# Kernel tuning notes

Hardware: AMD Instinct MI355X
Metric: run time of the kernel (lower is better)

## Reference

```python
import jax, jax.numpy as jnp
import numpy as np

K = 16
EPS = 1e-5

def _conv1x1(w, b, x):
    # w: [O, I], x: [B, I, N] -> [B, O, N]
    return jnp.einsum('oi,bin->bon', w, x) + b[None, :, None]

def _bn(g, be, m, v, x):
    # inference-mode batchnorm over channel dim of [B, C, N]
    inv = g / jnp.sqrt(v + EPS)
    return x * inv[None, :, None] + (be - m * inv)[None, :, None]

def setup_inputs() -> dict:
    key = jax.random.key(0)
    ks = jax.random.split(key, 16)
    B, C, N = 2, 128, 8192
    d = {}
    d['x'] = jax.random.normal(ks[0], (B, C, N), jnp.float32)
    d['xyz'] = jax.random.normal(ks[1], (B, N, 3), jnp.float32)
    def conv(k, o, i):
        k1, k2 = jax.random.split(k)
        s = 1.0 / np.sqrt(i)
        return (jax.random.uniform(k1, (o, i), jnp.float32, -s, s),
                jax.random.uniform(k2, (o,), jnp.float32, -s, s))
    def bn(k, c):
        return (jax.random.uniform(k, (c,), jnp.float32, 0.5, 1.5),
                jnp.zeros((c,), jnp.float32), jnp.zeros((c,), jnp.float32), jnp.ones((c,), jnp.float32))
    # boundary_net: 2C->C (bn,relu), C->C (bn,relu)
    d['bw1'], d['bb1'] = conv(ks[2], C, 2 * C)
    d['bn1g'], d['bn1b'], d['bn1m'], d['bn1v'] = bn(ks[3], C)
    d['bw2'], d['bb2'] = conv(ks[4], C, C)
    d['bn2g'], d['bn2b'], d['bn2m'], d['bn2v'] = bn(ks[5], C)
    # spatial_relation: 4->32 (bn,relu), 32->64
    d['sw1'], d['sb1'] = conv(ks[6], 32, 4)
    d['sbng'], d['sbnb'], d['sbnm'], d['sbnv'] = bn(ks[7], 32)
    d['sw2'], d['sb2'] = conv(ks[8], 64, 32)
    # attention: C+64 -> C//2 (bn,relu), C//2 -> C, sigmoid
    d['aw1'], d['ab1'] = conv(ks[9], C // 2, C + 64)
    d['abng'], d['abnb'], d['abnm'], d['abnv'] = bn(ks[10], C // 2)
    d['aw2'], d['ab2'] = conv(ks[11], C, C // 2)
    return d

def reference(x, xyz, bw1, bb1, bn1g, bn1b, bn1m, bn1v, bw2, bb2, bn2g, bn2b, bn2m, bn2v,
              sw1, sb1, sbng, sbnb, sbnm, sbnv, sw2, sb2,
              aw1, ab1, abng, abnb, abnm, abnv, aw2, ab2):
    B, C, N = x.shape
    # pairwise squared distances [B, N, N]
    xx = jnp.sum(xyz * xyz, axis=2)  # [B, N]
    dist = xx[:, :, None] + xx[:, None, :] - 2.0 * jnp.einsum('bnd,bmd->bnm', xyz, xyz)
    _, knn_idx = jax.lax.top_k(-dist, K)  # [B, N, K], K smallest distances
    # gather neighbor coords [B, N, K, 3]
    knn_xyz = jax.vmap(lambda p, i: p[i])(xyz, knn_idx)
    rel = knn_xyz - xyz[:, :, None, :]                  # [B, N, K, 3]
    rel_d = jnp.sqrt(jnp.sum(rel * rel, axis=-1))       # [B, N, K]
    mean_rel = jnp.mean(rel, axis=2).transpose(0, 2, 1)   # [B, 3, N]
    mean_d = jnp.mean(rel_d, axis=2)[:, None, :]           # [B, 1, N]
    spatial = jnp.concatenate([mean_rel, mean_d], axis=1)  # [B, 4, N]
    s = jax.nn.relu(_bn(sbng, sbnb, sbnm, sbnv, _conv1x1(sw1, sb1, spatial)))
    spatial_feat = _conv1x1(sw2, sb2, s)  # [B, 64, N]
    # gather neighbor features [B, C, N, K]
    knn_feat = jax.vmap(lambda xb, ib: xb[:, ib])(x, knn_idx)
    max_diff = jnp.max(knn_feat - x[:, :, :, None], axis=3)  # [B, C, N]
    bf = jnp.concatenate([x, max_diff], axis=1)  # [B, 2C, N]
    bf = jax.nn.relu(_bn(bn1g, bn1b, bn1m, bn1v, _conv1x1(bw1, bb1, bf)))
    boundary_feat = jax.nn.relu(_bn(bn2g, bn2b, bn2m, bn2v, _conv1x1(bw2, bb2, bf)))
    ai = jnp.concatenate([x, spatial_feat], axis=1)  # [B, C+64, N]
    a = jax.nn.relu(_bn(abng, abnb, abnm, abnv, _conv1x1(aw1, ab1, ai)))
    attn = jax.nn.sigmoid(_conv1x1(aw2, ab2, a))  # [B, C, N]
    return x + boundary_feat * attn
```

## Files before the change

kernel.cpp:

```cpp
#include <hip/hip_runtime.h>
#include <math.h>

#define NPTS  8192
#define NB    2
#define NTOT  (NPTS*NB)
#define GD    60
#define NCELL (GD*GD*GD)
#define TOTC  (NB*NCELL)
#define HCELL 0.2f
#define INVH  5.0f
#define ORGN  (-6.0f)
#define NN    8192
#define SCAN_CHUNK 1024
#define NBLK_SCAN  ((TOTC + SCAN_CHUNK - 1) / SCAN_CHUNK)
#define RSTART    2
#define RESC      4
#define SEL_CAP  1024

#define OFF_CNT     ((size_t)0)
#define OFF_OFFS    (OFF_CNT    + (size_t)TOTC*4)
#define OFF_CELLID  (OFF_OFFS   + (size_t)TOTC*4)
#define OFF_RANK    (OFF_CELLID + (size_t)NTOT*4)
#define OFF_SPOS    (OFF_RANK   + (size_t)NTOT*4)
#define OFF_KNN     (OFF_SPOS   + (size_t)NTOT*16)
#define OFF_SPATIAL (OFF_KNN    + (size_t)NTOT*16*4)
#define OFF_XT      (OFF_SPATIAL+ (size_t)NB*4*NPTS*4)
#define OFF_MD      (OFF_XT     + (size_t)NB*128*NPTS*4)
#define OFF_S1      (OFF_MD     + (size_t)NB*128*NPTS*4)
#define OFF_SF      (OFF_S1     + (size_t)NB*32*NPTS*4)
#define OFF_Y1      (OFF_SF     + (size_t)NB*64*NPTS*4)
#define OFF_Y2      (OFF_Y1     + (size_t)NB*128*NPTS*4)
#define OFF_A1      (OFF_Y2     + (size_t)NB*128*NPTS*4)
#define OFF_SC      (OFF_A1     + (size_t)NB*64*NPTS*4)
#define OFF_BSUM    (OFF_SC     + (size_t)1088*4)
#define OFF_BPRE    (OFF_BSUM   + (size_t)NBLK_SCAN*4)
#define OFF_RNG     (((OFF_BPRE + (size_t)NBLK_SCAN*4) + 15) & ~(size_t)15)

static __device__ __forceinline__ float sumsq3(float x, float y, float z) {
    return __fadd_rn(__fadd_rn(__fmul_rn(x, x), __fmul_rn(y, y)), __fmul_rn(z, z));
}
static __device__ __forceinline__ float pdist4(float qx, float qy, float qz, float qxx,
                                               float px, float py, float pz) {
    float pxx = sumsq3(px, py, pz);
    float dot = __fadd_rn(__fadd_rn(__fmul_rn(qx, px), __fmul_rn(qy, py)), __fmul_rn(qz, pz));
    return __fsub_rn(__fadd_rn(qxx, pxx), __fadd_rn(dot, dot));
}
static __device__ __forceinline__ unsigned fkey(float f) {
    unsigned b = __float_as_uint(f);
    return b ^ ((unsigned)(((int)b) >> 31) | 0x80000000u);
}
static __device__ __forceinline__ unsigned long long shflx64(unsigned long long v, int m) {
    unsigned lo = __shfl_xor((unsigned)v, m, 64);
    unsigned hi = __shfl_xor((unsigned)(v >> 32), m, 64);
    return ((unsigned long long)hi << 32) | lo;
}
static __device__ __forceinline__ int wave_scan_incl(int v, int lane) {
    #pragma unroll
    for (int d = 1; d < 64; d <<= 1) {
        int u = __shfl_up(v, d, 64);
        v += (lane >= d) ? u : 0;
    }
    return v;
}
static __device__ __forceinline__ unsigned long long tkmake(float m) {
    return ((unsigned long long)(fkey(__fsub_rn(__fmul_rn(m, m), 1e-4f)) + 1u)) << 27;
}

__global__ void cell_build(const float* __restrict__ xyz, int* __restrict__ cnt,
                           int* __restrict__ cellid, int* __restrict__ rank) {
    int t = blockIdx.x * 256 + threadIdx.x;
    if (t >= NTOT) return;
    const float* p = xyz + (size_t)t * 3;
    float x = p[0], y = p[1], z = p[2];
    int cx = min(GD - 1, max(0, (int)floorf((x - ORGN) * INVH)));
    int cy = min(GD - 1, max(0, (int)floorf((y - ORGN) * INVH)));
    int cz = min(GD - 1, max(0, (int)floorf((z - ORGN) * INVH)));
    int gcell = (t >> 13) * NCELL + (cz * GD + cy) * GD + cx;
    rank[t] = atomicAdd(&cnt[gcell], 1);
    cellid[t] = gcell;
}

__global__ __launch_bounds__(256) void scan_sums(const int* __restrict__ cnt, int* __restrict__ bsum) {
    __shared__ int red[256];
    int blk = blockIdx.x, t = threadIdx.x;
    int i0 = blk * SCAN_CHUNK + t * 4;
    int s = 0;
    if (i0 + 3 < TOTC) {
        int4 v = *(const int4*)(cnt + i0);
        s = v.x + v.y + v.z + v.w;
    } else {
        for (int j = 0; j < 4; ++j) if (i0 + j < TOTC) s += cnt[i0 + j];
    }
    red[t] = s;
    __syncthreads();
    for (int d = 128; d > 0; d >>= 1) {
        if (t < d) red[t] += red[t + d];
        __syncthreads();
    }
    if (t == 0) bsum[blk] = red[0];
}

__global__ __launch_bounds__(512) void scan_top(const int* __restrict__ bsum, int* __restrict__ bpre) {
    __shared__ int ps[512];
    int t = threadIdx.x;
    int v = (t < NBLK_SCAN) ? bsum[t] : 0;
    ps[t] = v;
    __syncthreads();
    for (int d = 1; d < 512; d <<= 1) {
        int u = 0;
        if (t >= d) u = ps[t - d];
        __syncthreads();
        ps[t] += u;
        __syncthreads();
    }
    if (t < NBLK_SCAN) bpre[t] = ps[t] - v;
}

__global__ __launch_bounds__(256) void scan_write(const int* __restrict__ cnt, const int* __restrict__ bpre,
                                                  int* __restrict__ offs, int2* __restrict__ rng) {
    __shared__ int ps[256];
    int blk = blockIdx.x, t = threadIdx.x;
    int i0 = blk * SCAN_CHUNK + t * 4;
    int a = 0, b = 0, c = 0, d = 0;
    if (i0 + 3 < TOTC) {
        int4 v = *(const int4*)(cnt + i0);
        a = v.x; b = v.y; c = v.z; d = v.w;
    } else {
        if (i0 + 0 < TOTC) a = cnt[i0 + 0];
        if (i0 + 1 < TOTC) b = cnt[i0 + 1];
        if (i0 + 2 < TOTC) c = cnt[i0 + 2];
        if (i0 + 3 < TOTC) d = cnt[i0 + 3];
    }
    int s = a + b + c + d;
    ps[t] = s;
    __syncthreads();
    for (int dd = 1; dd < 256; dd <<= 1) {
        int u = 0;
        if (t >= dd) u = ps[t - dd];
        __syncthreads();
        ps[t] += u;
        __syncthreads();
    }
    int base = bpre[blk] + ps[t] - s;
    if (i0 + 3 < TOTC) {
        offs[i0 + 0] = base;
        offs[i0 + 1] = base + a;
        offs[i0 + 2] = base + a + b;
        offs[i0 + 3] = base + a + b + c;
        *(int4*)(rng + i0)     = make_int4(base, base + a, base + a, base + a + b);
        *(int4*)(rng + i0 + 2) = make_int4(base + a + b, base + a + b + c,
                                           base + a + b + c, base + s);
    } else {
        if (i0 + 0 < TOTC) { offs[i0 + 0] = base;             rng[i0 + 0] = make_int2(base, base + a); }
        if (i0 + 1 < TOTC) { offs[i0 + 1] = base + a;         rng[i0 + 1] = make_int2(base + a, base + a + b); }
        if (i0 + 2 < TOTC) { offs[i0 + 2] = base + a + b;     rng[i0 + 2] = make_int2(base + a + b, base + a + b + c); }
        if (i0 + 3 < TOTC) { offs[i0 + 3] = base + a + b + c; rng[i0 + 3] = make_int2(base + a + b + c, base + s); }
    }
}

__global__ void scatter_k(const float* __restrict__ xyz, const int* __restrict__ cellid,
                          const int* __restrict__ rank, const int* __restrict__ offs,
                          float4* __restrict__ spos) {
    int t = blockIdx.x * 256 + threadIdx.x;
    if (t >= NTOT) return;
    const float* p = xyz + (size_t)t * 3;
    float x = p[0], y = p[1], z = p[2];
    int pos = offs[cellid[t]] + rank[t];
    spos[pos] = make_float4(x, y, z, __int_as_float(t & (NPTS - 1)));
}

__global__ __launch_bounds__(64) void knn_kernel(const float4* __restrict__ spos,
                                                 const int2* __restrict__ rng,
                                                 int* __restrict__ knn,
                                                 float* __restrict__ spatial) {
    __shared__ __align__(16) unsigned long long sel[SEL_CAP];
    __shared__ __align__(16) unsigned long long sel2[512];
    int lane = threadIdx.x;
    int bid  = blockIdx.x;
    int s = (bid & 7) * (NTOT / 8) + (bid >> 3);
    float4 q = spos[s];
    float qx = q.x, qy = q.y, qz = q.z;
    float qxx = sumsq3(qx, qy, qz);
    int b  = s >> 13;
    int nq = __float_as_int(q.w);
    int cx = min(GD - 1, max(0, (int)floorf((qx - ORGN) * INVH)));
    int cy = min(GD - 1, max(0, (int)floorf((qy - ORGN) * INVH)));
    int cz = min(GD - 1, max(0, (int)floorf((qz - ORGN) * INVH)));
    const int2* rg = rng + b * NCELL;

    float mlx = qx - (ORGN + (float)cx * HCELL);
    float mhx = (ORGN + (float)(cx + 1) * HCELL) - qx;
    float mly = qy - (ORGN + (float)cy * HCELL);
    float mhy = (ORGN + (float)(cy + 1) * HCELL) - qy;
    float mlz = qz - (ORGN + (float)cz * HCELL);
    float mhz = (ORGN + (float)(cz + 1) * HCELL) - qz;
    float margin0 = fminf(fminf(fminf(mlx, mhx), fminf(mly, mhy)), fminf(mlz, mhz));

    int tot = 0, ovf = 0;

    auto scan_ball = [&](int RB, float mfin, unsigned long long tkfin) {
        if (mfin <= 0.f) return;
        float mfin2 = mfin * mfin;
        int L = 2 * RB + 1, nrows = L * L;
        for (int r0 = 0; r0 < nrows; r0 += 64) {
            int nr = min(64, nrows - r0);
            int rr = r0 + lane;
            int num = 0, start = 0;
            if (rr < nrows) {
                int dzr = rr / L - RB, dyr = rr % L - RB;
                int zc = cz + dzr, yc = cy + dyr;
                if ((unsigned)zc < GD && (unsigned)yc < GD) {
                    float ylo = ORGN + (float)yc * HCELL;
                    float zlo = ORGN + (float)zc * HCELL;
                    float dyl = fmaxf(fmaxf(ylo - qy, qy - (ylo + HCELL)), 0.f);
                    float dzl = fmaxf(fmaxf(zlo - qz, qz - (zlo + HCELL)), 0.f);
                    float rem = mfin2 - dyl * dyl - dzl * dzl;
                    if (rem > -1e-4f) {
                        float xh = sqrtf(fmaxf(rem, 0.f)) + 1e-3f;
                        int xlo = max(0, (int)floorf((qx - xh - ORGN) * INVH));
                        int xhi = min(GD - 1, (int)floorf((qx + xh - ORGN) * INVH));
                        if (xlo <= xhi) {
                            int rowb = (zc * GD + yc) * GD;
                            start = rg[rowb + xlo].x;
                            num   = rg[rowb + xhi].y - start;
                        }
                    }
                }
            }
            int inc = wave_scan_incl(num, lane);
            int ctot = __shfl(inc, 63, 64);
            if (ctot == 0) continue;
            int excl = inc - num;
            auto eg = [&](int base, int& sv, float4& pv, bool& vld) {
                int t = base + lane;
                vld = t < ctot;
                int tc = vld ? t : (ctot - 1);
                int lo = 0, hi = nr - 1;
                #pragma unroll
                for (int st = 0; st < 6; ++st) {
                    int mid = (lo + hi + 1) >> 1;
                    int e = __shfl(excl, mid, 64);
                    bool g = (e <= tc);
                    lo = g ? mid : lo;
                    hi = g ? hi : (mid - 1);
                }
                sv = __shfl(start, lo, 64) + (tc - __shfl(excl, lo, 64));
                pv = spos[sv];
            };
            int s0; float4 p0; bool v0;
            eg(0, s0, p0, v0);
            for (int base = 0; base < ctot; base += 64) {
                int s1 = 0; float4 p1 = p0; bool v1 = false;
                if (base + 64 < ctot) eg(base + 64, s1, p1, v1);
                float d = pdist4(qx, qy, qz, qxx, p0.x, p0.y, p0.z);
                unsigned long long key = ((unsigned long long)fkey(d) << 27)
                                       | ((unsigned long long)(unsigned)__float_as_int(p0.w) << 14)
                                       | (unsigned)s0;
                bool pass = v0 && (key < tkfin);
                unsigned long long mk = __ballot(pass);
                int cnum = (int)__popcll(mk);
                if (tot + cnum > SEL_CAP) { ovf = 1; return; }
                if (pass) sel[tot + (int)__popcll(mk & ((1ULL << lane) - 1ULL))] = key;
                tot += cnum;
                s0 = s1; p0 = p1; v0 = v1;
            }
        }
    };

    auto count_below = [&](unsigned long long tk) {
        int c = 0;
        for (int t0 = 0; t0 < tot; t0 += 64) {
            int tt = t0 + lane;
            if (tt < tot) c += (sel[tt] < tk) ? 1 : 0;
        }
        for (int o = 32; o > 0; o >>= 1) c += __shfl_xor(c, o, 64);
        return c;
    };

    float mfin1 = margin0 + (float)RSTART * HCELL;
    unsigned long long tkf1 = (mfin1 > 0.f) ? tkmake(mfin1) : 0ULL;
    if (tkf1) scan_ball(RSTART, mfin1, tkf1);

    unsigned long long tkey_sel = ~0ULL;
    int csel = 0;
    bool have = false;
    if (!ovf && tot >= 16) {
        float mA = margin0 + 1.0f * HCELL;
        if (mA > 0.f) {
            unsigned long long tkA = tkmake(mA);
            int cA = count_below(tkA);
            if (cA >= 16) { tkey_sel = tkA; csel = cA; have = true; }
        }
        if (!have) { tkey_sel = ~0ULL; csel = tot; have = true; }
    }
    if (!have && !ovf) {
        tot = 0;
        float mfin4 = margin0 + (float)RESC * HCELL;
        unsigned long long tkf4 = (mfin4 > 0.f) ? tkmake(mfin4) : 0ULL;
        if (tkf4) scan_ball(RESC, mfin4, tkf4);
        if (!ovf && tot >= 16) {
            float mB = margin0 + (float)(RESC - 1) * HCELL;
            if (mB > 0.f) {
                unsigned long long tkB = tkmake(mB);
                int cB = count_below(tkB);
                if (cB >= 16) { tkey_sel = tkB; csel = cB; have = true; }
            }
            if (!have) { tkey_sel = ~0ULL; csel = tot; have = true; }
        }
    }

    if (!have) {
        const float LADR[16] = {0.35f, 0.4725f, 0.637875f, 0.86113125f,
                                1.1625272f, 1.5694117f, 2.1187058f, 2.8602529f,
                                3.8613414f, 5.2128109f, 7.0372947f, 9.5003478f,
                                12.825470f, 17.314384f, 23.374418f, 31.555464f};
        int sbase = b << 13;
        int cc[16];
        #pragma unroll
        for (int k = 0; k < 16; ++k) cc[k] = 0;
        for (int i0 = 0; i0 < NPTS; i0 += 64) {
            float4 p = spos[sbase + i0 + lane];
            float d = pdist4(qx, qy, qz, qxx, p.x, p.y, p.z);
            #pragma unroll
            for (int k = 0; k < 16; ++k) cc[k] += (d < LADR[k] * LADR[k]) ? 1 : 0;
        }
        #pragma unroll
        for (int k = 0; k < 16; ++k)
            for (int o = 32; o > 0; o >>= 1) cc[k] += __shfl_xor(cc[k], o, 64);
        float Tq = LADR[15] * LADR[15]; int cL = cc[15];
        #pragma unroll
        for (int k = 14; k >= 0; --k) if (cc[k] >= 16) { Tq = LADR[k] * LADR[k]; cL = cc[k]; }
        if (cL <= SEL_CAP) {
            tot = 0;
            for (int i0 = 0; i0 < NPTS; i0 += 64) {
                int idx = sbase + i0 + lane;
                float4 p = spos[idx];
                float d = pdist4(qx, qy, qz, qxx, p.x, p.y, p.z);
                bool pass = (d < Tq);
                unsigned long long key = ((unsigned long long)fkey(d) << 27)
                                       | ((unsigned long long)(unsigned)__float_as_int(p.w) << 14)
                                       | (unsigned)idx;
                unsigned long long mk = __ballot(pass);
                if (pass) sel[tot + (int)__popcll(mk & ((1ULL << lane) - 1ULL))] = key;
                tot += (int)__popcll(mk);
            }
            tkey_sel = ~0ULL;
            csel = tot;
        } else {
            unsigned long long* mybuf = sel + lane;
            unsigned long long minkey = ~0ULL, maxkey = 0;
            int nbuf = 0;
            for (int i = lane; i < NPTS; i += 64) {
                float4 p = spos[sbase + i];
                float d = pdist4(qx, qy, qz, qxx, p.x, p.y, p.z);
                unsigned long long key = ((unsigned long long)fkey(d) << 27)
                                       | ((unsigned long long)(unsigned)__float_as_int(p.w) << 14)
                                       | (unsigned)(sbase + i);
                if (nbuf < 16) {
                    mybuf[(size_t)nbuf * 64] = key;
                    ++nbuf;
                    minkey = (key < minkey) ? key : minkey;
                    maxkey = (key > maxkey) ? key : maxkey;
                } else if (key < maxkey) {
                    unsigned long long vmax = 0, v2 = 0;
                    int pmax = 0;
                    #pragma unroll
                    for (int j = 0; j < 16; ++j) {
                        unsigned long long v = mybuf[(size_t)j * 64];
                        if (v > vmax) { v2 = vmax; vmax = v; pmax = j; }
                        else if (v > v2) { v2 = v; }
                    }
                    mybuf[(size_t)pmax * 64] = key;
                    maxkey = (key > v2) ? key : v2;
                    minkey = (key < minkey) ? key : minkey;
                }
            }
            unsigned long long keep = ~0ULL;
            for (int k = 0; k < 16; ++k) {
                unsigned long long m = minkey;
                for (int o = 32; o > 0; o >>= 1) {
                    unsigned long long pv = shflx64(m, o);
                    m = (pv < m) ? pv : m;
                }
                unsigned long long bal = __ballot(minkey == m);
                int wl = __ffsll((long long)bal) - 1;
                if (lane == wl) {
                    int pos = 0;
                    for (int j = 0; j < nbuf; ++j) if (mybuf[(size_t)j * 64] == m) pos = j;
                    --nbuf;
                    mybuf[(size_t)pos * 64] = mybuf[(size_t)nbuf * 64];
                    unsigned long long nm = ~0ULL;
                    for (int j = 0; j < nbuf; ++j) {
                        unsigned long long v = mybuf[(size_t)j * 64];
                        nm = (v < nm) ? v : nm;
                    }
                    minkey = nm;
                }
                if (lane == k) keep = m;
            }
            float rx = 0.f, ry = 0.f, rz = 0.f, rd = 0.f;
            if (lane < 16) {
                int sp = (int)(keep & 0x3FFFu);
                int oi = (int)((keep >> 14) & 0x1FFFu);
                float4 p = spos[sp];
                rx = p.x - qx; ry = p.y - qy; rz = p.z - qz;
                rd = sqrtf(__fadd_rn(__fadd_rn(__fmul_rn(rx, rx), __fmul_rn(ry, ry)), __fmul_rn(rz, rz)));
                knn[(((size_t)b << 13) + nq) * 16 + lane] = oi;
            }
            for (int o = 8; o > 0; o >>= 1) {
                rx += __shfl_xor(rx, o, 64);
                ry += __shfl_xor(ry, o, 64);
                rz += __shfl_xor(rz, o, 64);
                rd += __shfl_xor(rd, o, 64);
            }
            if (lane == 0) {
                const float inv16 = 0.0625f;
                spatial[((size_t)b * 4 + 0) * NPTS + nq] = rx * inv16;
                spatial[((size_t)b * 4 + 1) * NPTS + nq] = ry * inv16;
                spatial[((size_t)b * 4 + 2) * NPTS + nq] = rz * inv16;
                spatial[((size_t)b * 4 + 3) * NPTS + nq] = rd * inv16;
            }
            return;
        }
    }

    const unsigned long long* src = sel;
    int m = tot;
    if (tkey_sel != ~0ULL && csel <= 512) {
        int w = 0;
        for (int t0 = 0; t0 < tot; t0 += 64) {
            int tt = t0 + lane;
            unsigned long long v = (tt < tot) ? sel[tt] : ~0ULL;
            bool pass = (tt < tot) && (v < tkey_sel);
            unsigned long long mk = __ballot(pass);
            if (pass) sel2[w + (int)__popcll(mk & ((1ULL << lane) - 1ULL))] = v;
            w += (int)__popcll(mk);
        }
        asm volatile("s_waitcnt lgkmcnt(0)" ::: "memory");
        __builtin_amdgcn_sched_barrier(0);
        src = sel2; m = w;
        tkey_sel = ~0ULL;
    }
    float rxs = 0.f, rys = 0.f, rzs = 0.f, rds = 0.f;
    for (int t0 = 0; t0 < m; t0 += 64) {
        int tt = t0 + lane;
        if (tt < m) {
            unsigned long long kt = src[tt];
            if (kt < tkey_sel) {
                int rr = 0;
                for (int j = 0; j < m; ++j) rr += (src[j] < kt) ? 1 : 0;
                if (rr < 16) {
                    int sp = (int)(kt & 0x3FFFu);
                    int oi = (int)((kt >> 14) & 0x1FFFu);
                    float4 p = spos[sp];
                    float dx = p.x - qx, dy = p.y - qy, dz = p.z - qz;
                    float dl = sqrtf(__fadd_rn(__fadd_rn(__fmul_rn(dx, dx), __fmul_rn(dy, dy)), __fmul_rn(dz, dz)));
                    knn[(((size_t)b << 13) + nq) * 16 + rr] = oi;
                    rxs += dx; rys += dy; rzs += dz; rds += dl;
                }
            }
        }
    }
    for (int o = 32; o > 0; o >>= 1) {
        rxs += __shfl_xor(rxs, o, 64);
        rys += __shfl_xor(rys, o, 64);
        rzs += __shfl_xor(rzs, o, 64);
        rds += __shfl_xor(rds, o, 64);
    }
    if (lane == 0) {
        const float inv16 = 0.0625f;
        spatial[((size_t)b * 4 + 0) * NPTS + nq] = rxs * inv16;
        spatial[((size_t)b * 4 + 1) * NPTS + nq] = rys * inv16;
        spatial[((size_t)b * 4 + 2) * NPTS + nq] = rzs * inv16;
        spatial[((size_t)b * 4 + 3) * NPTS + nq] = rds * inv16;
    }
}

__global__ void transpose_k(const float* __restrict__ x, float* __restrict__ xT) {
    __shared__ float tl[32][33];
    int b = blockIdx.z;
    int n0 = blockIdx.x * 32, c0 = blockIdx.y * 32;
    int tx = threadIdx.x, ty = threadIdx.y;
    const float* xb = x + (size_t)b * 128 * NN;
    float* xtb = xT + (size_t)b * NN * 128;
    for (int i = 0; i < 32; i += 8) tl[ty + i][tx] = xb[(size_t)(c0 + ty + i) * NN + n0 + tx];
    __syncthreads();
    for (int i = 0; i < 32; i += 8) xtb[(size_t)(n0 + ty + i) * 128 + c0 + tx] = tl[tx][ty + i];
}

__global__ __launch_bounds__(256) void md_k(const float* __restrict__ xT,
                                            const int* __restrict__ knn,
                                            float* __restrict__ md) {
    __shared__ int ki[8][16];
    __shared__ float smd[8][132];
    int b = blockIdx.y;
    int n0 = blockIdx.x * 8;
    int tid = threadIdx.x;
    if (tid < 128) ki[tid >> 4][tid & 15] = knn[(((size_t)b << 13) + n0 + (tid >> 4)) * 16 + (tid & 15)];
    __syncthreads();
    int nl = tid >> 5;
    int c4 = (tid & 31) * 4;
    const float* xb = xT + (size_t)b * NPTS * 128;
    float4 m = make_float4(-3.0e38f, -3.0e38f, -3.0e38f, -3.0e38f);
    #pragma unroll
    for (int k = 0; k < 16; ++k) {
        const float4 g = *(const float4*)(xb + (size_t)ki[nl][k] * 128 + c4);
        m.x = fmaxf(m.x, g.x); m.y = fmaxf(m.y, g.y); m.z = fmaxf(m.z, g.z); m.w = fmaxf(m.w, g.w);
    }
    const float4 own = *(const float4*)(xb + (size_t)(n0 + nl) * 128 + c4);
    m.x -= own.x; m.y -= own.y; m.z -= own.z; m.w -= own.w;
    *(float4*)(&smd[nl][c4]) = m;
    __syncthreads();
    for (int r = 0; r < 4; ++r) {
        int c = (tid >> 3) + 32 * r;
        int n2 = tid & 7;
        md[((size_t)b * 128 + c) * NN + n0 + n2] = smd[n2][c];
    }
}

__global__ void prep_k(const float* bb1, const float* g1, const float* be1, const float* m1, const float* v1,
                       const float* bb2, const float* g2, const float* be2, const float* m2, const float* v2,
                       const float* sb1, const float* gs,  const float* bes, const float* ms, const float* vs,
                       const float* sb2,
                       const float* ab1, const float* ga,  const float* bea, const float* ma, const float* va,
                       const float* ab2, float* sc) {
    int t = threadIdx.x;
    if (t < 128) {
        float i1 = g1[t] / sqrtf(v1[t] + 1e-5f);
        sc[t] = i1;        sc[128 + t] = bb1[t] * i1 + be1[t] - m1[t] * i1;
        float i2 = g2[t] / sqrtf(v2[t] + 1e-5f);
        sc[256 + t] = i2;  sc[384 + t] = bb2[t] * i2 + be2[t] - m2[t] * i2;
        sc[832 + t] = 1.0f; sc[960 + t] = ab2[t];
    }
    if (t < 32) {
        float is = gs[t] / sqrtf(vs[t] + 1e-5f);
        sc[512 + t] = is;  sc[544 + t] = sb1[t] * is + bes[t] - ms[t] * is;
    }
    if (t < 64) {
        sc[576 + t] = 1.0f; sc[640 + t] = sb2[t];
        float ia = ga[t] / sqrtf(va[t] + 1e-5f);
        sc[704 + t] = ia;  sc[768 + t] = ab1[t] * ia + bea[t] - ma[t] * ia;
    }
}

template <int O, int K, int TILE_N, int SPLIT, int ACT>
__global__ __launch_bounds__(256) void conv_bn(const float* __restrict__ srcA,
                                               const float* __restrict__ srcB,
                                               const float* __restrict__ W,
                                               const float* __restrict__ scale,
                                               const float* __restrict__ shift,
                                               float* __restrict__ out,
                                               const float* __restrict__ resx,
                                               const float* __restrict__ y2,
                                               float* __restrict__ dout) {
    constexpr int KC  = (K < 64) ? K : 64;
    constexpr int NT4 = TILE_N / 4;
    constexpr int O4  = O / 4;
    static_assert(NT4 * O4 == 256, "thread mapping");
    __shared__ float wT[KC][O + 4];
    __shared__ float inT[KC][TILE_N];
    int tid = threadIdx.x;
    int b = blockIdx.z;
    int n0 = blockIdx.x * TILE_N;
    int n_thr = tid % NT4;
    int o_thr = tid / NT4;
    float acc[4][4] = {{0.f, 0.f, 0.f, 0.f}, {0.f, 0.f, 0.f, 0.f}, {0.f, 0.f, 0.f, 0.f}, {0.f, 0.f, 0.f, 0.f}};

    for (int k0 = 0; k0 < K; k0 += KC) {
        for (int idx = tid; idx < KC * O; idx += 256) {
            int cc = idx % KC;
            int o  = idx / KC;
            wT[cc][o] = W[(size_t)o * K + k0 + cc];
        }
        for (int idx = tid; idx < KC * NT4; idx += 256) {
            int cc = idx / NT4;
            int nf = idx % NT4;
            int cg = k0 + cc;
            const float* src = (cg < SPLIT)
                ? (srcA + ((size_t)b * SPLIT + cg) * NN)
                : (srcB + ((size_t)b * (K - SPLIT) + (cg - SPLIT)) * NN);
            *(float4*)(&inT[cc][nf * 4]) = *(const float4*)(src + n0 + nf * 4);
        }
        __syncthreads();
        #pragma unroll 8
        for (int c = 0; c < KC; ++c) {
            float4 wv = *(const float4*)(&wT[c][o_thr * 4]);
            float4 iv = *(const float4*)(&inT[c][n_thr * 4]);
            acc[0][0] = fmaf(wv.x, iv.x, acc[0][0]); acc[0][1] = fmaf(wv.x, iv.y, acc[0][1]);
            acc[0][2] = fmaf(wv.x, iv.z, acc[0][2]); acc[0][3] = fmaf(wv.x, iv.w, acc[0][3]);
            acc[1][0] = fmaf(wv.y, iv.x, acc[1][0]); acc[1][1] = fmaf(wv.y, iv.y, acc[1][1]);
            acc[1][2] = fmaf(wv.y, iv.z, acc[1][2]); acc[1][3] = fmaf(wv.y, iv.w, acc[1][3]);
            acc[2][0] = fmaf(wv.z, iv.x, acc[2][0]); acc[2][1] = fmaf(wv.z, iv.y, acc[2][1]);
            acc[2][2] = fmaf(wv.z, iv.z, acc[2][2]); acc[2][3] = fmaf(wv.z, iv.w, acc[2][3]);
            acc[3][0] = fmaf(wv.w, iv.x, acc[3][0]); acc[3][1] = fmaf(wv.w, iv.y, acc[3][1]);
            acc[3][2] = fmaf(wv.w, iv.z, acc[3][2]); acc[3][3] = fmaf(wv.w, iv.w, acc[3][3]);
        }
        __syncthreads();
    }
    #pragma unroll
    for (int j = 0; j < 4; ++j) {
        int o = o_thr * 4 + j;
        float scv = scale[o], shv = shift[o];
        float4 v;
        v.x = fmaf(acc[j][0], scv, shv);
        v.y = fmaf(acc[j][1], scv, shv);
        v.z = fmaf(acc[j][2], scv, shv);
        v.w = fmaf(acc[j][3], scv, shv);
        size_t obase = ((size_t)b * O + o) * NN + n0 + n_thr * 4;
        if (ACT == 1) {
            v.x = fmaxf(v.x, 0.f); v.y = fmaxf(v.y, 0.f); v.z = fmaxf(v.z, 0.f); v.w = fmaxf(v.w, 0.f);
            *(float4*)(out + obase) = v;
        } else if (ACT == 2) {
            float4 xr = *(const float4*)(resx + obase);
            float4 yr = *(const float4*)(y2 + obase);
            v.x = xr.x + yr.x / (1.f + __expf(-v.x));
            v.y = xr.y + yr.y / (1.f + __expf(-v.y));
            v.z = xr.z + yr.z / (1.f + __expf(-v.z));
            v.w = xr.w + yr.w / (1.f + __expf(-v.w));
            *(float4*)(dout + obase) = v;
        } else {
            *(float4*)(out + obase) = v;
        }
    }
}

extern "C" void kernel_launch(void* const* d_in, const int* in_sizes, int n_in,
                              void* d_out, int out_size, void* d_ws, size_t ws_size,
                              hipStream_t stream) {
    (void)in_sizes; (void)n_in; (void)out_size; (void)ws_size;
    const float* x    = (const float*)d_in[0];
    const float* xyz  = (const float*)d_in[1];
    const float* bw1  = (const float*)d_in[2];
    const float* bb1  = (const float*)d_in[3];
    const float* bn1g = (const float*)d_in[4];
    const float* bn1b = (const float*)d_in[5];
    const float* bn1m = (const float*)d_in[6];
    const float* bn1v = (const float*)d_in[7];
    const float* bw2  = (const float*)d_in[8];
    const float* bb2  = (const float*)d_in[9];
    const float* bn2g = (const float*)d_in[10];
    const float* bn2b = (const float*)d_in[11];
    const float* bn2m = (const float*)d_in[12];
    const float* bn2v = (const float*)d_in[13];
    const float* sw1  = (const float*)d_in[14];
    const float* sb1  = (const float*)d_in[15];
    const float* sbng = (const float*)d_in[16];
    const float* sbnb = (const float*)d_in[17];
    const float* sbnm = (const float*)d_in[18];
    const float* sbnv = (const float*)d_in[19];
    const float* sw2  = (const float*)d_in[20];
    const float* sb2  = (const float*)d_in[21];
    const float* aw1  = (const float*)d_in[22];
    const float* ab1  = (const float*)d_in[23];
    const float* abng = (const float*)d_in[24];
    const float* abnb = (const float*)d_in[25];
    const float* abnm = (const float*)d_in[26];
    const float* abnv = (const float*)d_in[27];
    const float* aw2  = (const float*)d_in[28];
    const float* ab2  = (const float*)d_in[29];

    char* ws = (char*)d_ws;
    int*    cnt    = (int*)(ws + OFF_CNT);
    int*    offs   = (int*)(ws + OFF_OFFS);
    int*    cellid = (int*)(ws + OFF_CELLID);
    int*    rank   = (int*)(ws + OFF_RANK);
    float4* spos   = (float4*)(ws + OFF_SPOS);
    int*    knn    = (int*)(ws + OFF_KNN);
    float*  spat   = (float*)(ws + OFF_SPATIAL);
    float*  xT     = (float*)(ws + OFF_XT);
    float*  md     = (float*)(ws + OFF_MD);
    float*  s1b    = (float*)(ws + OFF_S1);
    float*  sfb    = (float*)(ws + OFF_SF);
    float*  y1b    = (float*)(ws + OFF_Y1);
    float*  y2b    = (float*)(ws + OFF_Y2);
    float*  a1b    = (float*)(ws + OFF_A1);
    float*  sc     = (float*)(ws + OFF_SC);
    int*    bsum   = (int*)(ws + OFF_BSUM);
    int*    bpre   = (int*)(ws + OFF_BPRE);
    int2*   rng    = (int2*)(ws + OFF_RNG);
    float*  dout   = (float*)d_out;

    hipMemsetAsync(cnt, 0, (size_t)TOTC * 4, stream);
    cell_build<<<dim3((NTOT + 255) / 256), 256, 0, stream>>>(xyz, cnt, cellid, rank);
    scan_sums<<<dim3(NBLK_SCAN), 256, 0, stream>>>(cnt, bsum);
    scan_top<<<dim3(1), 512, 0, stream>>>(bsum, bpre);
    scan_write<<<dim3(NBLK_SCAN), 256, 0, stream>>>(cnt, bpre, offs, rng);
    scatter_k<<<dim3((NTOT + 255) / 256), 256, 0, stream>>>(xyz, cellid, rank, offs, spos);
    knn_kernel<<<dim3(NTOT), 64, 0, stream>>>(spos, rng, knn, spat);
    transpose_k<<<dim3(NPTS / 32, 128 / 32, NB), dim3(32, 8), 0, stream>>>(x, xT);
    md_k<<<dim3(NPTS / 8, NB), 256, 0, stream>>>(xT, knn, md);
    prep_k<<<1, 128, 0, stream>>>(bb1, bn1g, bn1b, bn1m, bn1v,
                                  bb2, bn2g, bn2b, bn2m, bn2v,
                                  sb1, sbng, sbnb, sbnm, sbnv,
                                  sb2,
                                  ab1, abng, abnb, abnm, abnv,
                                  ab2, sc);
    conv_bn<32, 4, 128, 4, 1><<<dim3(NPTS / 128, 1, NB), 256, 0, stream>>>(
        spat, spat, sw1, sc + 512, sc + 544, s1b, nullptr, nullptr, nullptr);
    conv_bn<64, 32, 64, 32, 0><<<dim3(NPTS / 64, 1, NB), 256, 0, stream>>>(
        s1b, s1b, sw2, sc + 576, sc + 640, sfb, nullptr, nullptr, nullptr);
    conv_bn<128, 256, 32, 128, 1><<<dim3(NPTS / 32, 1, NB), 256, 0, stream>>>(
        x, md, bw1, sc + 0, sc + 128, y1b, nullptr, nullptr, nullptr);
    conv_bn<128, 128, 32, 128, 1><<<dim3(NPTS / 32, 1, NB), 256, 0, stream>>>(
        y1b, y1b, bw2, sc + 256, sc + 384, y2b, nullptr, nullptr, nullptr);
    conv_bn<64, 192, 64, 128, 1><<<dim3(NPTS / 64, 1, NB), 256, 0, stream>>>(
        x, sfb, aw1, sc + 704, sc + 768, a1b, nullptr, nullptr, nullptr);
    conv_bn<128, 64, 32, 64, 2><<<dim3(NPTS / 32, 1, NB), 256, 0, stream>>>(
        a1b, a1b, aw2, sc + 832, sc + 960, dout, x, y2b, dout);
}
```

Before: 326.0 us.

## Make knn kernel persistent and batch neighbor-cell loads four chunks at a time

The knn kernel becomes a grid-stride persistent loop over queries with a fixed 4096-block grid, replacing one block per query. Candidate loads are batched four 64-wide chunks at once to raise memory-level parallelism. The count of keys below the tighter threshold is now accumulated during the scan, removing a separate count_below pass over shared memory. The sel2 buffer is halved to 256 to cut shared memory and allow more resident waves, at the cost of a lower cutoff for the compaction step.

```diff
diff --git a/kernel.cpp b/kernel.cpp
--- a/kernel.cpp
+++ b/kernel.cpp
@@ -16,6 +16,7 @@
 #define RSTART    2
 #define RESC      4
 #define SEL_CAP  1024
+#define GRID_KNN 4096
 
 #define OFF_CNT     ((size_t)0)
 #define OFF_OFFS    (OFF_CNT    + (size_t)TOTC*4)
@@ -174,305 +175,312 @@
                                                  int* __restrict__ knn,
                                                  float* __restrict__ spatial) {
     __shared__ __align__(16) unsigned long long sel[SEL_CAP];
-    __shared__ __align__(16) unsigned long long sel2[512];
+    __shared__ __align__(16) unsigned long long sel2[256];
     int lane = threadIdx.x;
-    int bid  = blockIdx.x;
-    int s = (bid & 7) * (NTOT / 8) + (bid >> 3);
-    float4 q = spos[s];
-    float qx = q.x, qy = q.y, qz = q.z;
-    float qxx = sumsq3(qx, qy, qz);
-    int b  = s >> 13;
-    int nq = __float_as_int(q.w);
-    int cx = min(GD - 1, max(0, (int)floorf((qx - ORGN) * INVH)));
-    int cy = min(GD - 1, max(0, (int)floorf((qy - ORGN) * INVH)));
-    int cz = min(GD - 1, max(0, (int)floorf((qz - ORGN) * INVH)));
-    const int2* rg = rng + b * NCELL;
-
-    float mlx = qx - (ORGN + (float)cx * HCELL);
-    float mhx = (ORGN + (float)(cx + 1) * HCELL) - qx;
-    float mly = qy - (ORGN + (float)cy * HCELL);
-    float mhy = (ORGN + (float)(cy + 1) * HCELL) - qy;
-    float mlz = qz - (ORGN + (float)cz * HCELL);
-    float mhz = (ORGN + (float)(cz + 1) * HCELL) - qz;
-    float margin0 = fminf(fminf(fminf(mlx, mhx), fminf(mly, mhy)), fminf(mlz, mhz));
-
-    int tot = 0, ovf = 0;
-
-    auto scan_ball = [&](int RB, float mfin, unsigned long long tkfin) {
-        if (mfin <= 0.f) return;
-        float mfin2 = mfin * mfin;
-        int L = 2 * RB + 1, nrows = L * L;
-        for (int r0 = 0; r0 < nrows; r0 += 64) {
-            int nr = min(64, nrows - r0);
-            int rr = r0 + lane;
-            int num = 0, start = 0;
-            if (rr < nrows) {
-                int dzr = rr / L - RB, dyr = rr % L - RB;
-                int zc = cz + dzr, yc = cy + dyr;
-                if ((unsigned)zc < GD && (unsigned)yc < GD) {
-                    float ylo = ORGN + (float)yc * HCELL;
-                    float zlo = ORGN + (float)zc * HCELL;
-                    float dyl = fmaxf(fmaxf(ylo - qy, qy - (ylo + HCELL)), 0.f);
-                    float dzl = fmaxf(fmaxf(zlo - qz, qz - (zlo + HCELL)), 0.f);
-                    float rem = mfin2 - dyl * dyl - dzl * dzl;
-                    if (rem > -1e-4f) {
-                        float xh = sqrtf(fmaxf(rem, 0.f)) + 1e-3f;
-                        int xlo = max(0, (int)floorf((qx - xh - ORGN) * INVH));
-                        int xhi = min(GD - 1, (int)floorf((qx + xh - ORGN) * INVH));
-                        if (xlo <= xhi) {
-                            int rowb = (zc * GD + yc) * GD;
-                            start = rg[rowb + xlo].x;
-                            num   = rg[rowb + xhi].y - start;
+    for (int qi = blockIdx.x; qi < NTOT; qi += gridDim.x) {
+        int s = (qi & 7) * (NTOT / 8) + (qi >> 3);
+        float4 q = spos[s];
+        float qx = q.x, qy = q.y, qz = q.z;
+        float qxx = sumsq3(qx, qy, qz);
+        int b  = s >> 13;
+        int nq = __float_as_int(q.w);
+        int cx = min(GD - 1, max(0, (int)floorf((qx - ORGN) * INVH)));
+        int cy = min(GD - 1, max(0, (int)floorf((qy - ORGN) * INVH)));
+        int cz = min(GD - 1, max(0, (int)floorf((qz - ORGN) * INVH)));
+        const int2* rg = rng + b * NCELL;
+
+        float mlx = qx - (ORGN + (float)cx * HCELL);
+        float mhx = (ORGN + (float)(cx + 1) * HCELL) - qx;
+        float mly = qy - (ORGN + (float)cy * HCELL);
+        float mhy = (ORGN + (float)(cy + 1) * HCELL) - qy;
+        float mlz = qz - (ORGN + (float)cz * HCELL);
+        float mhz = (ORGN + (float)(cz + 1) * HCELL) - qz;
+        float margin0 = fminf(fminf(fminf(mlx, mhx), fminf(mly, mhy)), fminf(mlz, mhz));
+
+        int tot = 0, ovf = 0, cA = 0;
+        unsigned long long g_tkfin = 0, g_tkA = 0;
+
+        auto scan_ball = [&](int RB, float mfin) {
+            float mfin2 = mfin * mfin;
+            int L = 2 * RB + 1, nrows = L * L;
+            for (int r0 = 0; r0 < nrows && !ovf; r0 += 64) {
+                int nr = min(64, nrows - r0);
+                int rr = r0 + lane;
+                int num = 0, start = 0;
+                if (rr < nrows) {
+                    int dzr = rr / L - RB, dyr = rr % L - RB;
+                    int zc = cz + dzr, yc = cy + dyr;
+                    if ((unsigned)zc < GD && (unsigned)yc < GD) {
+                        float ylo = ORGN + (float)yc * HCELL;
+                        float zlo = ORGN + (float)zc * HCELL;
+                        float dyl = fmaxf(fmaxf(ylo - qy, qy - (ylo + HCELL)), 0.f);
+                        float dzl = fmaxf(fmaxf(zlo - qz, qz - (zlo + HCELL)), 0.f);
+                        float rem = mfin2 - dyl * dyl - dzl * dzl;
+                        if (rem > -1e-4f) {
+                            float xh = sqrtf(fmaxf(rem, 0.f)) + 1e-3f;
+                            int xlo = max(0, (int)floorf((qx - xh - ORGN) * INVH));
+                            int xhi = min(GD - 1, (int)floorf((qx + xh - ORGN) * INVH));
+                            if (xlo <= xhi) {
+                                int rowb = (zc * GD + yc) * GD;
+                                start = rg[rowb + xlo].x;
+                                num   = rg[rowb + xhi].y - start;
+                            }
                         }
                     }
                 }
+                int inc = wave_scan_incl(num, lane);
+                int ctot = __shfl(inc, 63, 64);
+                if (ctot == 0) continue;
+                int excl = inc - num;
+                int nch = (ctot + 63) >> 6;
+                auto srch = [&](int ck, int& sv, bool& vld) {
+                    int t = ck * 64 + lane;
+                    vld = t < ctot;
+                    int tc = vld ? t : (ctot - 1);
+                    int lo = 0, hi = nr - 1;
+                    #pragma unroll
+                    for (int st = 0; st < 6; ++st) {
+                        int mid = (lo + hi + 1) >> 1;
+                        int e = __shfl(excl, mid, 64);
+                        bool g = (e <= tc);
+                        lo = g ? mid : lo;
+                        hi = g ? hi : mid - 1;
+                    }
+                    sv = __shfl(start, lo, 64) + (tc - __shfl(excl, lo, 64));
+                };
+                auto proc = [&](int sv, float4 pv, bool vld) {
+                    if (ovf) return;
+                    float d = pdist4(qx, qy, qz, qxx, pv.x, pv.y, pv.z);
+                    unsigned long long key = ((unsigned long long)fkey(d) << 27)
+                                           | ((unsigned long long)(unsigned)__float_as_int(pv.w) << 14)
+                                           | (unsigned)sv;
+                    bool pass = vld && (key < g_tkfin);
+                    unsigned long long mk = __ballot(pass);
+                    int cnum = (int)__popcll(mk);
+                    if (tot + cnum > SEL_CAP) { ovf = 1; return; }
+                    if (pass) sel[tot + (int)__popcll(mk & ((1ULL << lane) - 1ULL))] = key;
+                    cA += (pass && key < g_tkA) ? 1 : 0;
+                    tot += cnum;
+                };
+                for (int cb = 0; cb < nch; cb += 4) {
+                    int s0 = 0, s1 = 0, s2 = 0, s3 = 0;
+                    bool v0 = false, v1 = false, v2 = false, v3 = false;
+                    float4 p0 = make_float4(0.f, 0.f, 0.f, 0.f);
+                    float4 p1 = p0, p2 = p0, p3 = p0;
+                    srch(cb, s0, v0); p0 = spos[s0];
+                    if (cb + 1 < nch) { srch(cb + 1, s1, v1); p1 = spos[s1]; }
+                    if (cb + 2 < nch) { srch(cb + 2, s2, v2); p2 = spos[s2]; }
+                    if (cb + 3 < nch) { srch(cb + 3, s3, v3); p3 = spos[s3]; }
+                    proc(s0, p0, v0);
+                    if (cb + 1 < nch) proc(s1, p1, v1);
+                    if (cb + 2 < nch) proc(s2, p2, v2);
+                    if (cb + 3 < nch) proc(s3, p3, v3);
+                    if (ovf) break;
+                }
             }
-            int inc = wave_scan_incl(num, lane);
-            int ctot = __shfl(inc, 63, 64);
-            if (ctot == 0) continue;
-            int excl = inc - num;
-            auto eg = [&](int base, int& sv, float4& pv, bool& vld) {
-                int t = base + lane;
-                vld = t < ctot;
-                int tc = vld ? t : (ctot - 1);
-                int lo = 0, hi = nr - 1;
+        };
+
+        float mfin1 = margin0 + (float)RSTART * HCELL;
+        if (mfin1 > 0.f) {
+            g_tkfin = tkmake(mfin1);
+            float mA = margin0 + 1.0f * HCELL;
+            g_tkA = (mA > 0.f) ? tkmake(mA) : 0ULL;
+            scan_ball(RSTART, mfin1);
+        }
+
+        unsigned long long tkey_sel = ~0ULL;
+        int csel = 0;
+        bool have = false;
+        if (!ovf && tot >= 16) {
+            int cAr = cA;
+            for (int o = 32; o > 0; o >>= 1) cAr += __shfl_xor(cAr, o, 64);
+            if (g_tkA != 0ULL && cAr >= 16) { tkey_sel = g_tkA; csel = cAr; }
+            else { tkey_sel = ~0ULL; csel = tot; }
+            have = true;
+        }
+        if (!have && !ovf) {
+            tot = 0; cA = 0;
+            float mfin4 = margin0 + (float)RESC * HCELL;
+            if (mfin4 > 0.f) {
+                g_tkfin = tkmake(mfin4);
+                float mB = margin0 + (float)(RESC - 1) * HCELL;
+                g_tkA = (mB > 0.f) ? tkmake(mB) : 0ULL;
+                scan_ball(RESC, mfin4);
+            }
+            if (!ovf && tot >= 16) {
+                int cBr = cA;
+                for (int o = 32; o > 0; o >>= 1) cBr += __shfl_xor(cBr, o, 64);
+                if (g_tkA != 0ULL && cBr >= 16) { tkey_sel = g_tkA; csel = cBr; }
+                else { tkey_sel = ~0ULL; csel = tot; }
+                have = true;
+            }
+        }
+
+        if (!have) {
+            const float LADR[16] = {0.35f, 0.4725f, 0.637875f, 0.86113125f,
+                                    1.1625272f, 1.5694117f, 2.1187058f, 2.8602529f,
+                                    3.8613414f, 5.2128109f, 7.0372947f, 9.5003478f,
+                                    12.825470f, 17.314384f, 23.374418f, 31.555464f};
+            int sbase = b << 13;
+            int cc[16];
+            #pragma unroll
+            for (int k = 0; k < 16; ++k) cc[k] = 0;
+            for (int i0 = 0; i0 < NPTS; i0 += 64) {
+                float4 p = spos[sbase + i0 + lane];
+                float d = pdist4(qx, qy, qz, qxx, p.x, p.y, p.z);
                 #pragma unroll
-                for (int st = 0; st < 6; ++st) {
-                    int mid = (lo + hi + 1) >> 1;
-                    int e = __shfl(excl, mid, 64);
-                    bool g = (e <= tc);
-                    lo = g ? mid : lo;
-                    hi = g ? hi : (mid - 1);
-                }
-                sv = __shfl(start, lo, 64) + (tc - __shfl(excl, lo, 64));
-                pv = spos[sv];
-            };
-            int s0; float4 p0; bool v0;
-            eg(0, s0, p0, v0);
-            for (int base = 0; base < ctot; base += 64) {
-                int s1 = 0; float4 p1 = p0; bool v1 = false;
-                if (base + 64 < ctot) eg(base + 64, s1, p1, v1);
-                float d = pdist4(qx, qy, qz, qxx, p0.x, p0.y, p0.z);
-                unsigned long long key = ((unsigned long long)fkey(d) << 27)
-                                       | ((unsigned long long)(unsigned)__float_as_int(p0.w) << 14)
-                                       | (unsigned)s0;
-                bool pass = v0 && (key < tkfin);
+                for (int k = 0; k < 16; ++k) cc[k] += (d < LADR[k] * LADR[k]) ? 1 : 0;
+            }
+            #pragma unroll
+            for (int k = 0; k < 16; ++k)
+                for (int o = 32; o > 0; o >>= 1) cc[k] += __shfl_xor(cc[k], o, 64);
+            float Tq = LADR[15] * LADR[15]; int cL = cc[15];
+            #pragma unroll
+            for (int k = 14; k >= 0; --k) if (cc[k] >= 16) { Tq = LADR[k] * LADR[k]; cL = cc[k]; }
+            if (cL <= SEL_CAP) {
+                tot = 0;
+                for (int i0 = 0; i0 < NPTS; i0 += 64) {
+                    int idx = sbase + i0 + lane;
+                    float4 p = spos[idx];
+                    float d = pdist4(qx, qy, qz, qxx, p.x, p.y, p.z);
+                    bool pass = (d < Tq);
+                    unsigned long long key = ((unsigned long long)fkey(d) << 27)
+                                           | ((unsigned long long)(unsigned)__float_as_int(p.w) << 14)
+                                           | (unsigned)idx;
+                    unsigned long long mk = __ballot(pass);
+                    if (pass) sel[tot + (int)__popcll(mk & ((1ULL << lane) - 1ULL))] = key;
+                    tot += (int)__popcll(mk);
+                }
+                tkey_sel = ~0ULL;
+                csel = tot;
+            } else {
+                unsigned long long* mybuf = sel + lane;
+                unsigned long long minkey = ~0ULL, maxkey = 0;
+                int nbuf = 0;
+                for (int i = lane; i < NPTS; i += 64) {
+                    float4 p = spos[sbase + i];
+                    float d = pdist4(qx, qy, qz, qxx, p.x, p.y, p.z);
+                    unsigned long long key = ((unsigned long long)fkey(d) << 27)
+                                           | ((unsigned long long)(unsigned)__float_as_int(p.w) << 14)
+                                           | (unsigned)(sbase + i);
+                    if (nbuf < 16) {
+                        mybuf[(size_t)nbuf * 64] = key;
+                        ++nbuf;
+                        minkey = (key < minkey) ? key : minkey;
+                        maxkey = (key > maxkey) ? key : maxkey;
+                    } else if (key < maxkey) {
+                        unsigned long long vmax = 0, v2 = 0;
+                        int pmax = 0;
+                        #pragma unroll
+                        for (int j = 0; j < 16; ++j) {
+                            unsigned long long v = mybuf[(size_t)j * 64];
+                            if (v > vmax) { v2 = vmax; vmax = v; pmax = j; }
+                            else if (v > v2) { v2 = v; }
+                        }
+                        mybuf[(size_t)pmax * 64] = key;
+                        maxkey = (key > v2) ? key : v2;
+                        minkey = (key < minkey) ? key : minkey;
+                    }
+                }
+                unsigned long long keep = ~0ULL;
+                for (int k = 0; k < 16; ++k) {
+                    unsigned long long m = minkey;
+                    for (int o = 32; o > 0; o >>= 1) {
+                        unsigned long long pv = shflx64(m, o);
+                        m = (pv < m) ? pv : m;
+                    }
+                    unsigned long long bal = __ballot(minkey == m);
+                    int wl = __ffsll((long long)bal) - 1;
+                    if (lane == wl) {
+                        int pos = 0;
+                        for (int j = 0; j < nbuf; ++j) if (mybuf[(size_t)j * 64] == m) pos = j;
+                        --nbuf;
+                        mybuf[(size_t)pos * 64] = mybuf[(size_t)nbuf * 64];
+                        unsigned long long nm = ~0ULL;
+                        for (int j = 0; j < nbuf; ++j) {
+                            unsigned long long v = mybuf[(size_t)j * 64];
+                            nm = (v < nm) ? v : nm;
+                        }
+                        minkey = nm;
+                    }
+                    if (lane == k) keep = m;
+                }
+                float rx = 0.f, ry = 0.f, rz = 0.f, rd = 0.f;
+                if (lane < 16) {
+                    int sp = (int)(keep & 0x3FFFu);
+                    int oi = (int)((keep >> 14) & 0x1FFFu);
+                    float4 p = spos[sp];
+                    rx = p.x - qx; ry = p.y - qy; rz = p.z - qz;
+                    rd = sqrtf(__fadd_rn(__fadd_rn(__fmul_rn(rx, rx), __fmul_rn(ry, ry)), __fmul_rn(rz, rz)));
+                    knn[(((size_t)b << 13) + nq) * 16 + lane] = oi;
+                }
+                for (int o = 8; o > 0; o >>= 1) {
+                    rx += __shfl_xor(rx, o, 64);
+                    ry += __shfl_xor(ry, o, 64);
+                    rz += __shfl_xor(rz, o, 64);
+                    rd += __shfl_xor(rd, o, 64);
+                }
+                if (lane == 0) {
+                    const float inv16 = 0.0625f;
+                    spatial[((size_t)b * 4 + 0) * NPTS + nq] = rx * inv16;
+                    spatial[((size_t)b * 4 + 1) * NPTS + nq] = ry * inv16;
+                    spatial[((size_t)b * 4 + 2) * NPTS + nq] = rz * inv16;
+                    spatial[((size_t)b * 4 + 3) * NPTS + nq] = rd * inv16;
+                }
+                continue;
+            }
+        }
+
+        const unsigned long long* src = sel;
+        int m = tot;
+        if (tkey_sel != ~0ULL && csel <= 256) {
+            int w = 0;
+            for (int t0 = 0; t0 < tot; t0 += 64) {
+                int tt = t0 + lane;
+                unsigned long long v = (tt < tot) ? sel[tt] : ~0ULL;
+                bool pass = (tt < tot) && (v < tkey_sel);
                 unsigned long long mk = __ballot(pass);
-                int cnum = (int)__popcll(mk);
-                if (tot + cnum > SEL_CAP) { ovf = 1; return; }
-                if (pass) sel[tot + (int)__popcll(mk & ((1ULL << lane) - 1ULL))] = key;
-                tot += cnum;
-                s0 = s1; p0 = p1; v0 = v1;
+                if (pass) sel2[w + (int)__popcll(mk & ((1ULL << lane) - 1ULL))] = v;
+                w += (int)__popcll(mk);
             }
-        }
-    };
-
-    auto count_below = [&](unsigned long long tk) {
-        int c = 0;
-        for (int t0 = 0; t0 < tot; t0 += 64) {
+            asm volatile("s_waitcnt lgkmcnt(0)" ::: "memory");
+            __builtin_amdgcn_sched_barrier(0);
+            src = sel2; m = w;
+            tkey_sel = ~0ULL;
+        }
+        float rxs = 0.f, rys = 0.f, rzs = 0.f, rds = 0.f;
+        for (int t0 = 0; t0 < m; t0 += 64) {
             int tt = t0 + lane;
-            if (tt < tot) c += (sel[tt] < tk) ? 1 : 0;
-        }
-        for (int o = 32; o > 0; o >>= 1) c += __shfl_xor(c, o, 64);
-        return c;
-    };
-
-    float mfin1 = margin0 + (float)RSTART * HCELL;
-    unsigned long long tkf1 = (mfin1 > 0.f) ? tkmake(mfin1) : 0ULL;
-    if (tkf1) scan_ball(RSTART, mfin1, tkf1);
-
-    unsigned long long tkey_sel = ~0ULL;
-    int csel = 0;
-    bool have = false;
-    if (!ovf && tot >= 16) {
-        float mA = margin0 + 1.0f * HCELL;
-        if (mA > 0.f) {
-            unsigned long long tkA = tkmake(mA);
-            int cA = count_below(tkA);
-            if (cA >= 16) { tkey_sel = tkA; csel = cA; have = true; }
-        }
-        if (!have) { tkey_sel = ~0ULL; csel = tot; have = true; }
-    }
-    if (!have && !ovf) {
-        tot = 0;
-        float mfin4 = margin0 + (float)RESC * HCELL;
-        unsigned long long tkf4 = (mfin4 > 0.f) ? tkmake(mfin4) : 0ULL;
-        if (tkf4) scan_ball(RESC, mfin4, tkf4);
-        if (!ovf && tot >= 16) {
-            float mB = margin0 + (float)(RESC - 1) * HCELL;
-            if (mB > 0.f) {
-                unsigned long long tkB = tkmake(mB);
-                int cB = count_below(tkB);
-                if (cB >= 16) { tkey_sel = tkB; csel = cB; have = true; }
+            if (tt < m) {
+                unsigned long long kt = src[tt];
+                if (kt < tkey_sel) {
+                    int rr = 0;
+                    for (int j = 0; j < m; ++j) rr += (src[j] < kt) ? 1 : 0;
+                    if (rr < 16) {
+                        int sp = (int)(kt & 0x3FFFu);
+                        int oi = (int)((kt >> 14) & 0x1FFFu);
+                        float4 p = spos[sp];
+                        float dx = p.x - qx, dy = p.y - qy, dz = p.z - qz;
+                        float dl = sqrtf(__fadd_rn(__fadd_rn(__fmul_rn(dx, dx), __fmul_rn(dy, dy)), __fmul_rn(dz, dz)));
+                        knn[(((size_t)b << 13) + nq) * 16 + rr] = oi;
+                        rxs += dx; rys += dy; rzs += dz; rds += dl;
+                    }
+                }
             }
-            if (!have) { tkey_sel = ~0ULL; csel = tot; have = true; }
-        }
-    }
-
-    if (!have) {
-        const float LADR[16] = {0.35f, 0.4725f, 0.637875f, 0.86113125f,
-                                1.1625272f, 1.5694117f, 2.1187058f, 2.8602529f,
-                                3.8613414f, 5.2128109f, 7.0372947f, 9.5003478f,
-                                12.825470f, 17.314384f, 23.374418f, 31.555464f};
-        int sbase = b << 13;
-        int cc[16];
-        #pragma unroll
-        for (int k = 0; k < 16; ++k) cc[k] = 0;
-        for (int i0 = 0; i0 < NPTS; i0 += 64) {
-            float4 p = spos[sbase + i0 + lane];
-            float d = pdist4(qx, qy, qz, qxx, p.x, p.y, p.z);
-            #pragma unroll
-            for (int k = 0; k < 16; ++k) cc[k] += (d < LADR[k] * LADR[k]) ? 1 : 0;
-        }
-        #pragma unroll
-        for (int k = 0; k < 16; ++k)
-            for (int o = 32; o > 0; o >>= 1) cc[k] += __shfl_xor(cc[k], o, 64);
-        float Tq = LADR[15] * LADR[15]; int cL = cc[15];
-        #pragma unroll
-        for (int k = 14; k >= 0; --k) if (cc[k] >= 16) { Tq = LADR[k] * LADR[k]; cL = cc[k]; }
-        if (cL <= SEL_CAP) {
-            tot = 0;
-            for (int i0 = 0; i0 < NPTS; i0 += 64) {
-                int idx = sbase + i0 + lane;
-                float4 p = spos[idx];
-                float d = pdist4(qx, qy, qz, qxx, p.x, p.y, p.z);
-                bool pass = (d < Tq);
-                unsigned long long key = ((unsigned long long)fkey(d) << 27)
-                                       | ((unsigned long long)(unsigned)__float_as_int(p.w) << 14)
-                                       | (unsigned)idx;
-                unsigned long long mk = __ballot(pass);
-                if (pass) sel[tot + (int)__popcll(mk & ((1ULL << lane) - 1ULL))] = key;
-                tot += (int)__popcll(mk);
-            }
-            tkey_sel = ~0ULL;
-            csel = tot;
-        } else {
-            unsigned long long* mybuf = sel + lane;
-            unsigned long long minkey = ~0ULL, maxkey = 0;
-            int nbuf = 0;
-            for (int i = lane; i < NPTS; i += 64) {
-                float4 p = spos[sbase + i];
-                float d = pdist4(qx, qy, qz, qxx, p.x, p.y, p.z);
-                unsigned long long key = ((unsigned long long)fkey(d) << 27)
-                                       | ((unsigned long long)(unsigned)__float_as_int(p.w) << 14)
-                                       | (unsigned)(sbase + i);
-                if (nbuf < 16) {
-                    mybuf[(size_t)nbuf * 64] = key;
-                    ++nbuf;
-                    minkey = (key < minkey) ? key : minkey;
-                    maxkey = (key > maxkey) ? key : maxkey;
-                } else if (key < maxkey) {
-                    unsigned long long vmax = 0, v2 = 0;
-                    int pmax = 0;
-                    #pragma unroll
-                    for (int j = 0; j < 16; ++j) {
-                        unsigned long long v = mybuf[(size_t)j * 64];
-                        if (v > vmax) { v2 = vmax; vmax = v; pmax = j; }
-                        else if (v > v2) { v2 = v; }
-                    }
-                    mybuf[(size_t)pmax * 64] = key;
-                    maxkey = (key > v2) ? key : v2;
-                    minkey = (key < minkey) ? key : minkey;
-                }
-            }
-            unsigned long long keep = ~0ULL;
-            for (int k = 0; k < 16; ++k) {
-                unsigned long long m = minkey;
-                for (int o = 32; o > 0; o >>= 1) {
-                    unsigned long long pv = shflx64(m, o);
-                    m = (pv < m) ? pv : m;
-                }
-                unsigned long long bal = __ballot(minkey == m);
-                int wl = __ffsll((long long)bal) - 1;
-                if (lane == wl) {
-                    int pos = 0;
-                    for (int j = 0; j < nbuf; ++j) if (mybuf[(size_t)j * 64] == m) pos = j;
-                    --nbuf;
-                    mybuf[(size_t)pos * 64] = mybuf[(size_t)nbuf * 64];
-                    unsigned long long nm = ~0ULL;
-                    for (int j = 0; j < nbuf; ++j) {
-                        unsigned long long v = mybuf[(size_t)j * 64];
-                        nm = (v < nm) ? v : nm;
-                    }
-                    minkey = nm;
-                }
-                if (lane == k) keep = m;
-            }
-            float rx = 0.f, ry = 0.f, rz = 0.f, rd = 0.f;
-            if (lane < 16) {
-                int sp = (int)(keep & 0x3FFFu);
-                int oi = (int)((keep >> 14) & 0x1FFFu);
-                float4 p = spos[sp];
-                rx = p.x - qx; ry = p.y - qy; rz = p.z - qz;
-                rd = sqrtf(__fadd_rn(__fadd_rn(__fmul_rn(rx, rx), __fmul_rn(ry, ry)), __fmul_rn(rz, rz)));
-                knn[(((size_t)b << 13) + nq) * 16 + lane] = oi;
-            }
-            for (int o = 8; o > 0; o >>= 1) {
-                rx += __shfl_xor(rx, o, 64);
-                ry += __shfl_xor(ry, o, 64);
-                rz += __shfl_xor(rz, o, 64);
-                rd += __shfl_xor(rd, o, 64);
-            }
-            if (lane == 0) {
-                const float inv16 = 0.0625f;
-                spatial[((size_t)b * 4 + 0) * NPTS + nq] = rx * inv16;
-                spatial[((size_t)b * 4 + 1) * NPTS + nq] = ry * inv16;
-                spatial[((size_t)b * 4 + 2) * NPTS + nq] = rz * inv16;
-                spatial[((size_t)b * 4 + 3) * NPTS + nq] = rd * inv16;
-            }
-            return;
-        }
-    }
-
-    const unsigned long long* src = sel;
-    int m = tot;
-    if (tkey_sel != ~0ULL && csel <= 512) {
-        int w = 0;
-        for (int t0 = 0; t0 < tot; t0 += 64) {
-            int tt = t0 + lane;
-            unsigned long long v = (tt < tot) ? sel[tt] : ~0ULL;
-            bool pass = (tt < tot) && (v < tkey_sel);
-            unsigned long long mk = __ballot(pass);
-            if (pass) sel2[w + (int)__popcll(mk & ((1ULL << lane) - 1ULL))] = v;
-            w += (int)__popcll(mk);
-        }
-        asm volatile("s_waitcnt lgkmcnt(0)" ::: "memory");
-        __builtin_amdgcn_sched_barrier(0);
-        src = sel2; m = w;
-        tkey_sel = ~0ULL;
-    }
-    float rxs = 0.f, rys = 0.f, rzs = 0.f, rds = 0.f;
-    for (int t0 = 0; t0 < m; t0 += 64) {
-        int tt = t0 + lane;
-        if (tt < m) {
-            unsigned long long kt = src[tt];
-            if (kt < tkey_sel) {
-                int rr = 0;
-                for (int j = 0; j < m; ++j) rr += (src[j] < kt) ? 1 : 0;
-                if (rr < 16) {
-                    int sp = (int)(kt & 0x3FFFu);
-                    int oi = (int)((kt >> 14) & 0x1FFFu);
-                    float4 p = spos[sp];
-                    float dx = p.x - qx, dy = p.y - qy, dz = p.z - qz;
-                    float dl = sqrtf(__fadd_rn(__fadd_rn(__fmul_rn(dx, dx), __fmul_rn(dy, dy)), __fmul_rn(dz, dz)));
-                    knn[(((size_t)b << 13) + nq) * 16 + rr] = oi;
-                    rxs += dx; rys += dy; rzs += dz; rds += dl;
-                }
-            }
-        }
-    }
-    for (int o = 32; o > 0; o >>= 1) {
-        rxs += __shfl_xor(rxs, o, 64);
-        rys += __shfl_xor(rys, o, 64);
-        rzs += __shfl_xor(rzs, o, 64);
-        rds += __shfl_xor(rds, o, 64);
-    }
-    if (lane == 0) {
-        const float inv16 = 0.0625f;
-        spatial[((size_t)b * 4 + 0) * NPTS + nq] = rxs * inv16;
-        spatial[((size_t)b * 4 + 1) * NPTS + nq] = rys * inv16;
-        spatial[((size_t)b * 4 + 2) * NPTS + nq] = rzs * inv16;
-        spatial[((size_t)b * 4 + 3) * NPTS + nq] = rds * inv16;
+        }
+        for (int o = 32; o > 0; o >>= 1) {
+            rxs += __shfl_xor(rxs, o, 64);
+            rys += __shfl_xor(rys, o, 64);
+            rzs += __shfl_xor(rzs, o, 64);
+            rds += __shfl_xor(rds, o, 64);
+        }
+        if (lane == 0) {
+            const float inv16 = 0.0625f;
+            spatial[((size_t)b * 4 + 0) * NPTS + nq] = rxs * inv16;
+            spatial[((size_t)b * 4 + 1) * NPTS + nq] = rys * inv16;
+            spatial[((size_t)b * 4 + 2) * NPTS + nq] = rzs * inv16;
+            spatial[((size_t)b * 4 + 3) * NPTS + nq] = rds * inv16;
+        }
     }
 }
 
@@ -686,7 +694,7 @@
     scan_top<<<dim3(1), 512, 0, stream>>>(bsum, bpre);
     scan_write<<<dim3(NBLK_SCAN), 256, 0, stream>>>(cnt, bpre, offs, rng);
     scatter_k<<<dim3((NTOT + 255) / 256), 256, 0, stream>>>(xyz, cellid, rank, offs, spos);
-    knn_kernel<<<dim3(NTOT), 64, 0, stream>>>(spos, rng, knn, spat);
+    knn_kernel<<<dim3(GRID_KNN), 64, 0, stream>>>(spos, rng, knn, spat);
     transpose_k<<<dim3(NPTS / 32, 128 / 32, NB), dim3(32, 8), 0, stream>>>(x, xT);
     md_k<<<dim3(NPTS / 8, NB), 256, 0, stream>>>(xT, knn, md);
     prep_k<<<1, 128, 0, stream>>>(bb1, bn1g, bn1b, bn1m, bn1v,
```

After: 350.3 us. +7.4%, slower.
